# Optimization experiments

Measured on AMD Instinct MI355X. Metric: run time of the kernel, lower is better.

## Reference

```python
import jax, jax.numpy as jnp
import numpy as np

V, E, H2, T = 50000, 512, 512, 9  # vocab, embed_dim, hidden per direction, n_tags
B, S = 64, 512
PAD = 0


def setup_inputs() -> dict:
    key = jax.random.key(0)
    ks = jax.random.split(key, 20)
    def n(k, shape, scale=0.1):
        return jax.random.normal(k, shape, dtype=jnp.float32) * scale
    sentence = jax.random.randint(ks[0], (B, S), 0, V, dtype=jnp.int32)
    tags = jax.random.randint(ks[1], (B, S), 0, T, dtype=jnp.int32)
    emb = n(ks[2], (V, E)).at[PAD].set(0.0)  # padding_idx row is zero
    w_ih_f, w_hh_f = n(ks[3], (4 * H2, E)), n(ks[4], (4 * H2, H2))
    b_ih_f, b_hh_f = n(ks[5], (4 * H2,)), n(ks[6], (4 * H2,))
    w_ih_b, w_hh_b = n(ks[7], (4 * H2, E)), n(ks[8], (4 * H2, H2))
    b_ih_b, b_hh_b = n(ks[9], (4 * H2,)), n(ks[10], (4 * H2,))
    w_lin, b_lin = n(ks[11], (T, 2 * H2)), n(ks[12], (T,))
    start_trans, end_trans, trans = n(ks[13], (T,)), n(ks[14], (T,)), n(ks[15], (T, T))
    h0 = jax.random.normal(ks[16], (2, B, H2), dtype=jnp.float32)  # torch.randn init hidden
    c0 = jax.random.normal(ks[17], (2, B, H2), dtype=jnp.float32)
    return dict(sentence=sentence, tags=tags, emb=emb,
                w_ih_f=w_ih_f, w_hh_f=w_hh_f, b_ih_f=b_ih_f, b_hh_f=b_hh_f,
                w_ih_b=w_ih_b, w_hh_b=w_hh_b, b_ih_b=b_ih_b, b_hh_b=b_hh_b,
                w_lin=w_lin, b_lin=b_lin,
                start_trans=start_trans, end_trans=end_trans, trans=trans,
                h0=h0, c0=c0)


def _lstm_dir(x, w_ih, w_hh, b_ih, b_hh, h, c):
    # x: (S, B, E). PyTorch gate order: i, f, g, o.
    bias = b_ih + b_hh
    def step(carry, xt):
        h, c = carry
        g = xt @ w_ih.T + h @ w_hh.T + bias
        i, f, gg, o = jnp.split(g, 4, axis=-1)
        c = jax.nn.sigmoid(f) * c + jax.nn.sigmoid(i) * jnp.tanh(gg)
        h = jax.nn.sigmoid(o) * jnp.tanh(c)
        return (h, c), h
    _, hs = jax.lax.scan(step, (h, c), x)
    return hs  # (S, B, H2)


def reference(sentence, tags, emb, w_ih_f, w_hh_f, b_ih_f, b_hh_f,
              w_ih_b, w_hh_b, b_ih_b, b_hh_b, w_lin, b_lin,
              start_trans, end_trans, trans, h0, c0):
    x = emb[sentence].transpose(1, 0, 2)  # (S, B, E)
    hf = _lstm_dir(x, w_ih_f, w_hh_f, b_ih_f, b_hh_f, h0[0], c0[0])
    hb = _lstm_dir(x[::-1], w_ih_b, w_hh_b, b_ih_b, b_hh_b, h0[1], c0[1])[::-1]
    out = jnp.concatenate([hf, hb], axis=-1)  # (S, B, 2*H2)
    em = (out @ w_lin.T + b_lin).transpose(1, 0, 2)  # (B, S, T) emissions

    tags = tags.astype(jnp.int32)
    # --- numerator: score of gold path (full mask) ---
    em_sc = jnp.take_along_axis(em, tags[:, :, None], axis=2)[..., 0]  # (B, S)
    num = (start_trans[tags[:, 0]] + em_sc.sum(axis=1)
           + trans[tags[:, :-1], tags[:, 1:]].sum(axis=1)
           + end_trans[tags[:, -1]])  # (B,)

    # --- denominator: forward algorithm (log partition) ---
    alpha0 = start_trans[None, :] + em[:, 0]  # (B, T)
    rest = em[:, 1:].transpose(1, 0, 2)  # (S-1, B, T)
    def step(a, e):
        # a: (B, T) log-alpha; broadcast over next tag j: a_i + trans_ij + e_j
        nxt = jax.nn.logsumexp(a[:, :, None] + trans[None, :, :] + e[:, None, :], axis=1)
        return nxt, None
    alpha, _ = jax.lax.scan(step, alpha0, rest)
    denom = jax.nn.logsumexp(alpha + end_trans[None, :], axis=-1)  # (B,)

    # torchcrf reduction='mean' is mean over batch; module returns -llh
    return -jnp.mean(num - denom)
```

## Files before the change

### kernel.cpp

```cpp
#include <hip/hip_runtime.h>
#include <hip/hip_bf16.h>
#include <cstdint>
#include <cstddef>


typedef __attribute__((ext_vector_type(4))) float f32x4;
typedef __attribute__((ext_vector_type(8))) short bf16x8;

#define DEVINL __device__ __forceinline__

static constexpr size_t XWR_OFF  = 0;
static constexpr size_t X_OFF    = 268435456;
static constexpr size_t HS_OFF   = 301989888;
static constexpr size_t WIH_OFF  = 369098752;
static constexpr size_t WHH_OFF  = 373293056;
static constexpr size_t BIAS_OFF = 377487360;
static constexpr size_t H_OFF    = 377503744;
static constexpr size_t EM_OFF   = 377765888;

DEVINL unsigned short f2bf(float f) {
  unsigned u = __builtin_bit_cast(unsigned, f);
  unsigned r = u + 0x7fffu + ((u >> 16) & 1u);
  return (unsigned short)(r >> 16);
}
DEVINL float bf2f(unsigned int h) {
  unsigned u = (h & 0xffffu) << 16;
  return __builtin_bit_cast(float, u);
}
DEVINL bf16x8 as_bf16x8(uint4 v) { return __builtin_bit_cast(bf16x8, v); }

DEVINL float fsigmoid(float x) {
  const float e = exp2f(-1.4426950408889634f * x);
  return __builtin_amdgcn_rcpf(1.f + e);
}
DEVINL float ftanh(float x) {
  const float e = exp2f(2.8853900817779268f * x);
  return 1.f - 2.f * __builtin_amdgcn_rcpf(e + 1.f);
}
DEVINL float selbf(uint2 v, int r) {
  const unsigned u = (r < 2) ? v.x : v.y;
  return bf2f((r & 1) ? (u >> 16) : u);
}

__global__ void k_gather(const int* __restrict__ sent, const float* __restrict__ emb,
                         unsigned short* __restrict__ x) {
  const int m = blockIdx.x;
  const int s = m >> 6, b = m & 63;
  const int tok = sent[b * 512 + s];
  const float4 v = ((const float4*)(emb + (size_t)tok * 512))[threadIdx.x];
  uint2 o;
  o.x = (unsigned)f2bf(v.x) | ((unsigned)f2bf(v.y) << 16);
  o.y = (unsigned)f2bf(v.z) | ((unsigned)f2bf(v.w) << 16);
  ((uint2*)(x + (size_t)m * 512))[threadIdx.x] = o;
}

__global__ void k_prep(const float* __restrict__ wihf, const float* __restrict__ whhf,
                       const float* __restrict__ bihf, const float* __restrict__ bhhf,
                       const float* __restrict__ wihb, const float* __restrict__ whhb,
                       const float* __restrict__ bihb, const float* __restrict__ bhhb,
                       unsigned short* __restrict__ Wih, unsigned short* __restrict__ Whh,
                       float* __restrict__ bias) {
  const int n = blockIdx.x;
  const int dir = n >> 11, r = n & 2047;
  const float* wi = dir ? wihb : wihf;
  const float* wh = dir ? whhb : whhf;
  const float4 a = ((const float4*)(wi + (size_t)r * 512))[threadIdx.x];
  const float4 c = ((const float4*)(wh + (size_t)r * 512))[threadIdx.x];
  uint2 oa, oc;
  oa.x = (unsigned)f2bf(a.x) | ((unsigned)f2bf(a.y) << 16);
  oa.y = (unsigned)f2bf(a.z) | ((unsigned)f2bf(a.w) << 16);
  oc.x = (unsigned)f2bf(c.x) | ((unsigned)f2bf(c.y) << 16);
  oc.y = (unsigned)f2bf(c.z) | ((unsigned)f2bf(c.w) << 16);
  ((uint2*)(Wih + (size_t)n * 512))[threadIdx.x] = oa;
  ((uint2*)(Whh + (size_t)n * 512))[threadIdx.x] = oc;
  if (threadIdx.x == 0)
    bias[n] = dir ? (bihb[r] + bhhb[r]) : (bihf[r] + bhhf[r]);
}

__global__ void k_inith(const float* __restrict__ h0, unsigned short* __restrict__ hg) {
  const int gi = blockIdx.x * 256 + threadIdx.x;
  const int dir = gi >> 13, rem = gi & 8191;
  const int row = rem >> 7, c = rem & 127;
  const int slot = c >> 2, off = (c & 3) * 4;
  const float4 v = *(const float4*)(h0 + ((size_t)(dir * 64 + row)) * 512 + slot * 16 + off);
  const unsigned long long p =
      (unsigned long long)f2bf(v.x) | ((unsigned long long)f2bf(v.y) << 16) |
      ((unsigned long long)f2bf(v.z) << 32) | ((unsigned long long)f2bf(v.w) << 48);
  __hip_atomic_store(
      (unsigned long long*)(hg + (((size_t)dir * 32 + slot) * 64 + row) * 16 + off),
      p, __ATOMIC_RELAXED, __HIP_MEMORY_SCOPE_AGENT);
}

typedef __attribute__((address_space(1))) const unsigned int* as1c_u32p;
typedef __attribute__((address_space(3))) unsigned int* as3_u32p;

DEVINL void async16(const void* g, void* l) {
  __builtin_amdgcn_global_load_lds((as1c_u32p)g, (as3_u32p)l, 16, 0, 0);
}

__global__ __launch_bounds__(256) void k_gemm(const unsigned short* __restrict__ X,
                                              const unsigned short* __restrict__ W,
                                              const float* __restrict__ bias,
                                              unsigned short* __restrict__ XWr) {
  __shared__ unsigned short Asm[8192];
  __shared__ unsigned short Bsm[8192];
  const int nt = blockIdx.x, mt = blockIdx.y;
  const int tid = threadIdx.x, lane = tid & 63, w = tid >> 6;
  const int wm = w & 1, wn = w >> 1;
  const int ul = lane & 15, q = lane >> 4;
  const int srow = lane >> 3, schunk = lane & 7;

  f32x4 acc[4][4];
  const f32x4 fz = {0.f, 0.f, 0.f, 0.f};
#pragma unroll
  for (int i = 0; i < 4; i++)
#pragma unroll
    for (int j = 0; j < 4; j++) acc[i][j] = fz;

  for (int k0 = 0; k0 < 512; k0 += 64) {
    __syncthreads();
#pragma unroll
    for (int rep = 0; rep < 4; rep++) {
      const int row = rep * 32 + w * 8 + srow;
      const int ca = (schunk ^ (row & 7)) << 3;
      async16(X + (size_t)(mt * 128 + row) * 512 + k0 + ca, Asm + (rep * 32 + w * 8) * 64);
      async16(W + (size_t)(nt * 128 + row) * 512 + k0 + ca, Bsm + (rep * 32 + w * 8) * 64);
    }
    __syncthreads();
#pragma unroll
    for (int kk = 0; kk < 2; kk++) {
      bf16x8 af[4], bfr[4];
#pragma unroll
      for (int i = 0; i < 4; i++) {
        const int ra = wm * 64 + i * 16 + ul;
        const int pa = (kk * 4 + q) ^ (ra & 7);
        af[i] = *(const bf16x8*)(Asm + ra * 64 + pa * 8);
        const int rb = wn * 64 + i * 16 + ul;
        const int pb = (kk * 4 + q) ^ (rb & 7);
        bfr[i] = *(const bf16x8*)(Bsm + rb * 64 + pb * 8);
      }
#pragma unroll
      for (int i = 0; i < 4; i++)
#pragma unroll
        for (int j = 0; j < 4; j++)
          acc[i][j] = __builtin_amdgcn_mfma_f32_16x16x32_bf16(af[i], bfr[j], acc[i][j], 0, 0, 0);
    }
  }

  const int s = mt * 2 + wm;
  const int nb = nt * 128 + wn * 64;
#pragma unroll
  for (int j = 0; j < 4; j++) {
    const int n = nb + j * 16;
    const int dir = n >> 11, g = (n >> 9) & 3, slot = (n >> 4) & 31;
    const float bs = bias[n + ul];
#pragma unroll
    for (int i = 0; i < 4; i++) {
      const f32x4 v = acc[i][j];
      uint2 o;
      o.x = (unsigned)f2bf(v[0] + bs) | ((unsigned)f2bf(v[1] + bs) << 16);
      o.y = (unsigned)f2bf(v[2] + bs) | ((unsigned)f2bf(v[3] + bs) << 16);
      const size_t idx = ((((((size_t)s * 2 + dir) * 32 + slot) * 4 + g) * 4 + i) * 64 + lane) * 4;
      *(uint2*)(XWr + idx) = o;
    }
  }
}

__global__ __launch_bounds__(256, 1) void k_lstm(const unsigned short* __restrict__ Whh,
                                                 const unsigned short* __restrict__ XWr,
                                                 const float* __restrict__ c0,
                                                 unsigned short* __restrict__ hg,
                                                 unsigned short* __restrict__ hs,
                                                 unsigned int* __restrict__ tags) {
  __shared__ uint4 wlds[4096];
  __shared__ __align__(16) unsigned short hstage[4][320];
  const int tid = threadIdx.x, lane = tid & 63, wv = tid >> 6;
  const int dir = blockIdx.x >> 5, slot = blockIdx.x & 31;
  const int u0 = slot << 4;
  const int ul = lane & 15, q = lane >> 4;
  const int b_base = wv << 4;
  const int rlocal = lane >> 2, chunk = lane & 3;

#pragma unroll
  for (int i = 0; i < 16; i++) {
    const int f = i * 4 + wv;
    const int g = f & 3, kk = f >> 2;
    const int row = dir * 2048 + g * 512 + u0 + ul;
    wlds[f * 64 + lane] = *(const uint4*)(Whh + (size_t)row * 512 + kk * 32 + q * 8);
  }

  float c[4];
#pragma unroll
  for (int r = 0; r < 4; r++)
    c[r] = c0[((size_t)dir * 64 + b_base + q * 4 + r) * 512 + u0 + ul];

  unsigned int* mytag = tags + (((size_t)dir * 4 + wv) * 32 + slot) * 32;
  const unsigned int* ptag = tags + ((size_t)dir * 4 + wv) * 32 * 32;

  uint2 xg[4];
  {
    const int tt0 = dir ? 511 : 0;
#pragma unroll
    for (int g = 0; g < 4; g++)
      xg[g] = *(const uint2*)(XWr + (size_t)tt0 * 262144 +
                              (((((size_t)dir * 32 + slot) * 4 + g) * 4 + wv) * 64 + lane) * 4);
  }

  __syncthreads();

  for (int t = 0; t < 512; t++) {
    const int tt = dir ? (511 - t) : t;
    const size_t rbase = ((size_t)(t & 1) * 2 + dir) * 32768;

    unsigned long long ha[32];
#pragma unroll
    for (int kk = 0; kk < 16; kk++) {
      const int slotS = 2 * kk + (q >> 1);
      const unsigned long long* p = (const unsigned long long*)
          (hg + rbase + ((size_t)slotS * 64 + b_base + ul) * 16 + (q & 1) * 8);
      ha[2 * kk]     = __hip_atomic_load(p,     __ATOMIC_RELAXED, __HIP_MEMORY_SCOPE_AGENT);
      ha[2 * kk + 1] = __hip_atomic_load(p + 1, __ATOMIC_RELAXED, __HIP_MEMORY_SCOPE_AGENT);
    }

    uint2 xgn[4];
    if (t < 511) {
      const int ttn = dir ? (511 - (t + 1)) : (t + 1);
#pragma unroll
      for (int g = 0; g < 4; g++)
        xgn[g] = *(const uint2*)(XWr + (size_t)ttn * 262144 +
                                 (((((size_t)dir * 32 + slot) * 4 + g) * 4 + wv) * 64 + lane) * 4);
    }

    f32x4 acc[4];
    const f32x4 fz = {0.f, 0.f, 0.f, 0.f};
    acc[0] = fz; acc[1] = fz; acc[2] = fz; acc[3] = fz;
#pragma unroll
    for (int kk = 0; kk < 16; kk++) {
      uint4 av;
      av.x = (unsigned)ha[2 * kk];
      av.y = (unsigned)(ha[2 * kk] >> 32);
      av.z = (unsigned)ha[2 * kk + 1];
      av.w = (unsigned)(ha[2 * kk + 1] >> 32);
      const bf16x8 a8 = as_bf16x8(av);
#pragma unroll
      for (int g = 0; g < 4; g++) {
        const bf16x8 b8 = as_bf16x8(wlds[(kk * 4 + g) * 64 + lane]);
        acc[g] = __builtin_amdgcn_mfma_f32_16x16x32_bf16(a8, b8, acc[g], 0, 0, 0);
      }
    }

#pragma unroll
    for (int r = 0; r < 4; r++) {
      const float gi = acc[0][r] + selbf(xg[0], r);
      const float gf = acc[1][r] + selbf(xg[1], r);
      const float gg = acc[2][r] + selbf(xg[2], r);
      const float go = acc[3][r] + selbf(xg[3], r);
      const float i_ = fsigmoid(gi);
      const float f_ = fsigmoid(gf);
      const float g_ = ftanh(gg);
      const float o_ = fsigmoid(go);
      c[r] = f_ * c[r] + i_ * g_;
      const float h = o_ * ftanh(c[r]);
      hstage[wv][(q * 4 + r) * 20 + ul] = f2bf(h);
    }

    asm volatile("" ::: "memory");

    unsigned long long v;
    __builtin_memcpy(&v, &hstage[wv][rlocal * 20 + chunk * 4], 8);

    *(unsigned long long*)(hs + ((size_t)tt * 64 + b_base + rlocal) * 1024 +
                           dir * 512 + u0 + chunk * 4) = v;

    if (t < 511) {
      const size_t wbase = ((size_t)((t & 1) ^ 1) * 2 + dir) * 32768;
      __hip_atomic_store(
          (unsigned long long*)(hg + wbase + ((size_t)slot * 64 + b_base + rlocal) * 16 + chunk * 4),
          v, __ATOMIC_RELAXED, __HIP_MEMORY_SCOPE_AGENT);
      asm volatile("s_waitcnt vmcnt(0)" ::: "memory");
      if (lane == 0)
        __hip_atomic_store(mytag, (unsigned)(t + 1), __ATOMIC_RELAXED,
                           __HIP_MEMORY_SCOPE_AGENT);

      const unsigned target = (unsigned)(t + 1);
      int spins = 0;
      for (;;) {
        unsigned tg = 0xFFFFFFFFu;
        if (lane < 32)
          tg = __hip_atomic_load(ptag + (size_t)lane * 32, __ATOMIC_RELAXED,
                                 __HIP_MEMORY_SCOPE_AGENT);
        if (__all(tg >= target)) break;
        if (++spins > 3000000) break;
      }
      xg[0] = xgn[0]; xg[1] = xgn[1]; xg[2] = xgn[2]; xg[3] = xgn[3];
    }
  }
}

DEVINL void unpack8(uint4 v, float* o) {
  o[0] = bf2f(v.x); o[1] = bf2f(v.x >> 16);
  o[2] = bf2f(v.y); o[3] = bf2f(v.y >> 16);
  o[4] = bf2f(v.z); o[5] = bf2f(v.z >> 16);
  o[6] = bf2f(v.w); o[7] = bf2f(v.w >> 16);
}

__global__ __launch_bounds__(256) void k_emis(const unsigned short* __restrict__ hs,
                                              const float* __restrict__ wlin,
                                              const float* __restrict__ blin,
                                              float* __restrict__ em) {
  const int lane = threadIdx.x & 63, wv = threadIdx.x >> 6;
  const int p = blockIdx.x * 4 + wv;
  const int s = p >> 6, b = p & 63;
  const uint4* row = (const uint4*)(hs + (size_t)p * 1024);
  const uint4 v0 = row[lane * 2], v1 = row[lane * 2 + 1];
  float hv[16];
  unpack8(v0, hv);
  unpack8(v1, hv + 8);
#pragma unroll 1
  for (int tag = 0; tag < 9; tag++) {
    const float4* wr = (const float4*)(wlin + (size_t)tag * 1024 + lane * 16);
    float sum = 0.f;
#pragma unroll
    for (int jj = 0; jj < 4; jj++) {
      const float4 w4 = wr[jj];
      sum += hv[jj * 4 + 0] * w4.x + hv[jj * 4 + 1] * w4.y +
             hv[jj * 4 + 2] * w4.z + hv[jj * 4 + 3] * w4.w;
    }
#pragma unroll
    for (int off = 32; off > 0; off >>= 1) sum += __shfl_down(sum, off);
    if (lane == 0) em[((size_t)b * 512 + s) * 9 + tag] = sum + blin[tag];
  }
}

__global__ void k_crf(const float* __restrict__ em, const int* __restrict__ tags,
                      const float* __restrict__ st, const float* __restrict__ et,
                      const float* __restrict__ tr, float* __restrict__ loss) {
  const int b = blockIdx.x, lane = threadIdx.x;
  const float L2E = 1.4426950408889634f, LN2 = 0.6931471805599453f;

  float np = 0.f;
  for (int s = lane; s < 512; s += 64) {
    const int tg = tags[b * 512 + s];
    np += em[((size_t)b * 512 + s) * 9 + tg];
    if (s > 0) np += tr[tags[b * 512 + s - 1] * 9 + tg];
  }
#pragma unroll
  for (int off = 32; off > 0; off >>= 1) np += __shfl_down(np, off);

  const int j = (lane < 9) ? lane : 0;
  float tcol[9];
#pragma unroll
  for (int i = 0; i < 9; i++) tcol[i] = tr[i * 9 + j];
  float alpha = st[j] + em[((size_t)b * 512 + 0) * 9 + j];
  for (int s = 1; s < 512; s++) {
    float abc[9];
#pragma unroll
    for (int i = 0; i < 9; i++) abc[i] = __shfl(alpha, i) + tcol[i];
    float mx = abc[0];
#pragma unroll
    for (int i = 1; i < 9; i++) mx = fmaxf(mx, abc[i]);
    float sm = 0.f;
#pragma unroll
    for (int i = 0; i < 9; i++) sm += exp2f((abc[i] - mx) * L2E);
    alpha = mx + log2f(sm) * LN2 + em[((size_t)b * 512 + s) * 9 + j];
  }
  float v = (lane < 9) ? (alpha + et[j]) : -3.0e38f;
  float mx = v;
#pragma unroll
  for (int off = 32; off > 0; off >>= 1) mx = fmaxf(mx, __shfl_xor(mx, off));
  float se = (lane < 9) ? exp2f((v - mx) * L2E) : 0.f;
#pragma unroll
  for (int off = 32; off > 0; off >>= 1) se += __shfl_xor(se, off);
  const float denom = mx + log2f(se) * LN2;

  if (lane == 0) {
    const float num = np + st[tags[b * 512]] + et[tags[b * 512 + 511]];
    atomicAdd(loss, num - denom);
  }
}

__global__ void k_final(const float* __restrict__ loss, float* __restrict__ out) {
  out[0] = -loss[0] * (1.f / 64.f);
}

extern "C" void kernel_launch(void* const* d_in, const int* in_sizes, int n_in,
                              void* d_out, int out_size, void* d_ws, size_t ws_size,
                              hipStream_t stream) {
  (void)in_sizes; (void)n_in; (void)out_size; (void)ws_size;
  const int*   sentence = (const int*)d_in[0];
  const int*   tags     = (const int*)d_in[1];
  const float* emb      = (const float*)d_in[2];
  const float* w_ih_f   = (const float*)d_in[3];
  const float* w_hh_f   = (const float*)d_in[4];
  const float* b_ih_f   = (const float*)d_in[5];
  const float* b_hh_f   = (const float*)d_in[6];
  const float* w_ih_b   = (const float*)d_in[7];
  const float* w_hh_b   = (const float*)d_in[8];
  const float* b_ih_b   = (const float*)d_in[9];
  const float* b_hh_b   = (const float*)d_in[10];
  const float* w_lin    = (const float*)d_in[11];
  const float* b_lin    = (const float*)d_in[12];
  const float* start_t  = (const float*)d_in[13];
  const float* end_t    = (const float*)d_in[14];
  const float* trans    = (const float*)d_in[15];
  const float* h0       = (const float*)d_in[16];
  const float* c0       = (const float*)d_in[17];

  char* ws = (char*)d_ws;
  unsigned short* XWr = (unsigned short*)(ws + XWR_OFF);
  unsigned short* X   = (unsigned short*)(ws + X_OFF);
  unsigned short* HS  = (unsigned short*)(ws + HS_OFF);
  unsigned short* WIH = (unsigned short*)(ws + WIH_OFF);
  unsigned short* WHH = (unsigned short*)(ws + WHH_OFF);
  float*          BIAS= (float*)(ws + BIAS_OFF);
  unsigned short* HG  = (unsigned short*)(ws + H_OFF);
  float*          EM  = (float*)(ws + EM_OFF);
  unsigned int*   TAGS= (unsigned int*)(ws + X_OFF);
  float*          LOSS= (float*)(ws + X_OFF + 32768);

  k_gather<<<32768, 128, 0, stream>>>(sentence, emb, X);
  k_prep<<<4096, 128, 0, stream>>>(w_ih_f, w_hh_f, b_ih_f, b_hh_f,
                                   w_ih_b, w_hh_b, b_ih_b, b_hh_b, WIH, WHH, BIAS);
  k_inith<<<64, 256, 0, stream>>>(h0, HG);
  k_gemm<<<dim3(32, 256), 256, 0, stream>>>(X, WIH, BIAS, XWr);
  hipMemsetAsync(TAGS, 0, 32768 + 64, stream);
  k_lstm<<<64, 256, 0, stream>>>(WHH, XWr, c0, HG, HS, TAGS);
  k_emis<<<8192, 256, 0, stream>>>(HS, w_lin, b_lin, EM);
  k_crf<<<64, 64, 0, stream>>>(EM, tags, start_t, end_t, trans, LOSS);
  k_final<<<1, 1, 0, stream>>>(LOSS, (float*)d_out);
}
```

Before: 2.840 ms.

## Replace LSTM per-step tag barrier with sentinel-flagged 4-deep hidden-state ring

Drops the per-step flag-and-barrier handshake in the persistent LSTM kernel. Each step's hidden state now goes into a 4-slot ring buffer pre-filled with a sentinel bf16 pattern, and consumers poll the data itself until no sentinel remains. Each wave re-poisons the slot it consumed. This removes the vmcnt drain, the separate tag store and the all-to-all tag poll, so producers and consumers synchronise only on the data they need. The risk is that a legitimate hidden value could equal the sentinel pattern 0x7F7F; that pattern is about 3.4e38 in bf16, which h cannot reach because it is bounded by tanh. The ring is also moved into the former tag region of the workspace.

Result: faster. 2.462 ms (-13.3%).

```diff
diff --git a/kernel.cpp b/kernel.cpp
--- a/kernel.cpp
+++ b/kernel.cpp
@@ -15,7 +15,6 @@
 static constexpr size_t WIH_OFF  = 369098752;
 static constexpr size_t WHH_OFF  = 373293056;
 static constexpr size_t BIAS_OFF = 377487360;
-static constexpr size_t H_OFF    = 377503744;
 static constexpr size_t EM_OFF   = 377765888;
 
 DEVINL unsigned short f2bf(float f) {
@@ -86,9 +85,14 @@
   const unsigned long long p =
       (unsigned long long)f2bf(v.x) | ((unsigned long long)f2bf(v.y) << 16) |
       ((unsigned long long)f2bf(v.z) << 32) | ((unsigned long long)f2bf(v.w) << 48);
-  __hip_atomic_store(
-      (unsigned long long*)(hg + (((size_t)dir * 32 + slot) * 64 + row) * 16 + off),
-      p, __ATOMIC_RELAXED, __HIP_MEMORY_SCOPE_AGENT);
+  const size_t base = (((size_t)dir * 32 + slot) * 64 + row) * 16 + off;
+  __hip_atomic_store((unsigned long long*)(hg + base), p,
+                     __ATOMIC_RELAXED, __HIP_MEMORY_SCOPE_AGENT);
+  const unsigned long long CAN = 0x7F7F7F7F7F7F7F7FULL;
+#pragma unroll
+  for (int b = 1; b < 4; b++)
+    __hip_atomic_store((unsigned long long*)(hg + (size_t)b * 65536 + base), CAN,
+                       __ATOMIC_RELAXED, __HIP_MEMORY_SCOPE_AGENT);
 }
 
 typedef __attribute__((address_space(1))) const unsigned int* as1c_u32p;
@@ -170,8 +174,7 @@
                                                  const unsigned short* __restrict__ XWr,
                                                  const float* __restrict__ c0,
                                                  unsigned short* __restrict__ hg,
-                                                 unsigned short* __restrict__ hs,
-                                                 unsigned int* __restrict__ tags) {
+                                                 unsigned short* __restrict__ hs) {
   __shared__ uint4 wlds[4096];
   __shared__ __align__(16) unsigned short hstage[4][320];
   const int tid = threadIdx.x, lane = tid & 63, wv = tid >> 6;
@@ -180,6 +183,7 @@
   const int ul = lane & 15, q = lane >> 4;
   const int b_base = wv << 4;
   const int rlocal = lane >> 2, chunk = lane & 3;
+  const unsigned long long CAN = 0x7F7F7F7F7F7F7F7FULL;
 
 #pragma unroll
   for (int i = 0; i < 16; i++) {
@@ -194,9 +198,6 @@
   for (int r = 0; r < 4; r++)
     c[r] = c0[((size_t)dir * 64 + b_base + q * 4 + r) * 512 + u0 + ul];
 
-  unsigned int* mytag = tags + (((size_t)dir * 4 + wv) * 32 + slot) * 32;
-  const unsigned int* ptag = tags + ((size_t)dir * 4 + wv) * 32 * 32;
-
   uint2 xg[4];
   {
     const int tt0 = dir ? 511 : 0;
@@ -210,25 +211,33 @@
 
   for (int t = 0; t < 512; t++) {
     const int tt = dir ? (511 - t) : t;
-    const size_t rbase = ((size_t)(t & 1) * 2 + dir) * 32768;
+    const size_t rbase = ((size_t)(t & 3) * 2 + dir) * 32768;
 
     unsigned long long ha[32];
-#pragma unroll
-    for (int kk = 0; kk < 16; kk++) {
-      const int slotS = 2 * kk + (q >> 1);
-      const unsigned long long* p = (const unsigned long long*)
-          (hg + rbase + ((size_t)slotS * 64 + b_base + ul) * 16 + (q & 1) * 8);
-      ha[2 * kk]     = __hip_atomic_load(p,     __ATOMIC_RELAXED, __HIP_MEMORY_SCOPE_AGENT);
-      ha[2 * kk + 1] = __hip_atomic_load(p + 1, __ATOMIC_RELAXED, __HIP_MEMORY_SCOPE_AGENT);
-    }
-
-    uint2 xgn[4];
-    if (t < 511) {
-      const int ttn = dir ? (511 - (t + 1)) : (t + 1);
-#pragma unroll
-      for (int g = 0; g < 4; g++)
-        xgn[g] = *(const uint2*)(XWr + (size_t)ttn * 262144 +
-                                 (((((size_t)dir * 32 + slot) * 4 + g) * 4 + wv) * 64 + lane) * 4);
+    int rounds = 0;
+    for (;;) {
+      unsigned bad = 0;
+#pragma unroll
+      for (int kk = 0; kk < 16; kk++) {
+        const int slotS = 2 * kk + (q >> 1);
+        const unsigned long long* p = (const unsigned long long*)
+            (hg + rbase + ((size_t)slotS * 64 + b_base + ul) * 16 + (q & 1) * 8);
+        ha[2 * kk]     = __hip_atomic_load(p,     __ATOMIC_RELAXED, __HIP_MEMORY_SCOPE_AGENT);
+        ha[2 * kk + 1] = __hip_atomic_load(p + 1, __ATOMIC_RELAXED, __HIP_MEMORY_SCOPE_AGENT);
+      }
+#pragma unroll
+      for (int i = 0; i < 32; i++)
+        bad |= (((unsigned)ha[i] & 0xFFFFu) == 0x7F7Fu) ? 1u : 0u;
+      if (__all(bad == 0)) break;
+      if (++rounds > 2000000) break;
+      __builtin_amdgcn_s_sleep(1);
+    }
+
+    if (t >= 1) {
+      __hip_atomic_store(
+          (unsigned long long*)(hg + ((size_t)((t - 1) & 3) * 2 + dir) * 32768 +
+                                ((size_t)slot * 64 + b_base + rlocal) * 16 + chunk * 4),
+          CAN, __ATOMIC_RELAXED, __HIP_MEMORY_SCOPE_AGENT);
     }
 
     f32x4 acc[4];
@@ -269,30 +278,21 @@
     unsigned long long v;
     __builtin_memcpy(&v, &hstage[wv][rlocal * 20 + chunk * 4], 8);
 
-    *(unsigned long long*)(hs + ((size_t)tt * 64 + b_base + rlocal) * 1024 +
-                           dir * 512 + u0 + chunk * 4) = v;
-
     if (t < 511) {
-      const size_t wbase = ((size_t)((t & 1) ^ 1) * 2 + dir) * 32768;
+      const size_t wbase = ((size_t)((t + 1) & 3) * 2 + dir) * 32768;
       __hip_atomic_store(
           (unsigned long long*)(hg + wbase + ((size_t)slot * 64 + b_base + rlocal) * 16 + chunk * 4),
           v, __ATOMIC_RELAXED, __HIP_MEMORY_SCOPE_AGENT);
-      asm volatile("s_waitcnt vmcnt(0)" ::: "memory");
-      if (lane == 0)
-        __hip_atomic_store(mytag, (unsigned)(t + 1), __ATOMIC_RELAXED,
-                           __HIP_MEMORY_SCOPE_AGENT);
-
-      const unsigned target = (unsigned)(t + 1);
-      int spins = 0;
-      for (;;) {
-        unsigned tg = 0xFFFFFFFFu;
-        if (lane < 32)
-          tg = __hip_atomic_load(ptag + (size_t)lane * 32, __ATOMIC_RELAXED,
-                                 __HIP_MEMORY_SCOPE_AGENT);
-        if (__all(tg >= target)) break;
-        if (++spins > 3000000) break;
-      }
-      xg[0] = xgn[0]; xg[1] = xgn[1]; xg[2] = xgn[2]; xg[3] = xgn[3];
+    }
+    *(unsigned long long*)(hs + ((size_t)tt * 64 + b_base + rlocal) * 1024 +
+                           dir * 512 + u0 + chunk * 4) = v;
+
+    if (t < 511) {
+      const int ttn = dir ? (511 - (t + 1)) : (t + 1);
+#pragma unroll
+      for (int g = 0; g < 4; g++)
+        xg[g] = *(const uint2*)(XWr + (size_t)ttn * 262144 +
+                                (((((size_t)dir * 32 + slot) * 4 + g) * 4 + wv) * 64 + lane) * 4);
     }
   }
 }
@@ -413,18 +413,17 @@
   unsigned short* WIH = (unsigned short*)(ws + WIH_OFF);
   unsigned short* WHH = (unsigned short*)(ws + WHH_OFF);
   float*          BIAS= (float*)(ws + BIAS_OFF);
-  unsigned short* HG  = (unsigned short*)(ws + H_OFF);
   float*          EM  = (float*)(ws + EM_OFF);
-  unsigned int*   TAGS= (unsigned int*)(ws + X_OFF);
-  float*          LOSS= (float*)(ws + X_OFF + 32768);
+  float*          LOSS= (float*)(ws + X_OFF);
+  unsigned short* HG4 = (unsigned short*)(ws + X_OFF + 4096);
 
   k_gather<<<32768, 128, 0, stream>>>(sentence, emb, X);
   k_prep<<<4096, 128, 0, stream>>>(w_ih_f, w_hh_f, b_ih_f, b_hh_f,
                                    w_ih_b, w_hh_b, b_ih_b, b_hh_b, WIH, WHH, BIAS);
-  k_inith<<<64, 256, 0, stream>>>(h0, HG);
   k_gemm<<<dim3(32, 256), 256, 0, stream>>>(X, WIH, BIAS, XWr);
-  hipMemsetAsync(TAGS, 0, 32768 + 64, stream);
-  k_lstm<<<64, 256, 0, stream>>>(WHH, XWr, c0, HG, HS, TAGS);
+  hipMemsetAsync(LOSS, 0, 64, stream);
+  k_inith<<<64, 256, 0, stream>>>(h0, HG4);
+  k_lstm<<<64, 256, 0, stream>>>(WHH, XWr, c0, HG4, HS);
   k_emis<<<8192, 256, 0, stream>>>(HS, w_lin, b_lin, EM);
   k_crf<<<64, 64, 0, stream>>>(EM, tags, start_t, end_t, trans, LOSS);
   k_final<<<1, 1, 0, stream>>>(LOSS, (float*)d_out);
```
